# Kernel optimization log

Measured on AMD Instinct MI355X. Metric: run time of the kernel, lower is better.

## Reference

```python
import math
import jax, jax.numpy as jnp
import numpy as np

# ---- module hyperparameters (from init_kwargs) ----
MAX_DISP = 48
IMG_WIDTH = 1248
W = IMG_WIDTH // 4          # 312 rows of the OT problem (left pixels)
C_COLS = MAX_DISP + W       # 360 columns (shifted right pixels)
NUM_ITER = 10
TAU = 0.95
EPS = 1.0
KAPPA = (1.0 - TAU) / 2.0
XI = (1.0 - TAU) / (1.0 + TAU)
RHO = EPS * TAU / (1.0 - TAU)
BIG_COST = 10000.0

B, H = 2, 64


def setup_inputs() -> dict:
    key = jax.random.key(0)
    scores = jax.random.normal(key, (B, MAX_DISP, H, W), dtype=jnp.float32)
    return {"scores": scores}


def _masked(x):
    # torch.where(isfinite(x), x, 0)
    return jnp.where(jnp.isfinite(x), x, jnp.zeros_like(x))


def _lse_kernel(Cm, f, g, axis):
    # S = (C - f[...,None] - g[...,None,:]) / eps ; eps*logsumexp(-S, axis)
    S = (Cm - f[..., None] - g[..., None, :]) / EPS
    w_res = EPS * jax.nn.logsumexp(-S, axis=axis)
    w_sgn = f if axis == -1 else g
    return w_res - _masked(w_sgn)


def _sinkhorn_update(Cm, f, g, axis, log_marginal):
    app = _lse_kernel(Cm, f, g, axis)
    return EPS * log_marginal - _masked(app)


def _smin(h, log_marginal):
    return -RHO * jax.nn.logsumexp(-h / RHO + log_marginal, axis=-1)


def _unbalanced_ot(Cm):
    # Cm: (B,H,W,C_COLS) cost matrix
    log_a = jnp.full((W,), -math.log(W), dtype=Cm.dtype)
    log_b = jnp.full((C_COLS,), -math.log(C_COLS), dtype=Cm.dtype)

    f = -EPS * jax.nn.logsumexp(-Cm / EPS + log_b, axis=-1)          # (B,H,W)
    g = jnp.zeros(Cm.shape[:2] + (C_COLS,), dtype=Cm.dtype)          # (B,H,C)

    for _ in range(NUM_ITER):
        old_f = f
        new_g = TAU * _sinkhorn_update(Cm, old_f, g, axis=-2, log_marginal=log_b)
        new_g = new_g - KAPPA * _smin(old_f, log_a)[..., None]
        new_g = new_g + XI * _smin(new_g, log_b)[..., None]
        new_f = TAU * _sinkhorn_update(Cm, f, new_g, axis=-1, log_marginal=log_a)
        new_f = new_f - KAPPA * _smin(new_g, log_b)[..., None]
        new_f = new_f + XI * _smin(new_f, log_a)[..., None]
        f, g = new_f, new_g

    S = (Cm - f[..., None] - g[..., None, :]) / EPS
    return jnp.exp(-S)                                               # transport plan P


def _scatter_to_cost(scores):
    # (B,D,H,W) scores -> (B,H,W,C_COLS) cost, vectorized scatter over d
    Bn, D, Hn, Wn = scores.shape
    j = jnp.arange(Wn)
    d = jnp.arange(D)
    col = j[None, :] - d[:, None] + MAX_DISP                          # (D,W), all in-range, no collisions
    jj = jnp.broadcast_to(j[None, :], (D, Wn))
    cost = jnp.full((Bn, Hn, Wn, C_COLS), BIG_COST, dtype=scores.dtype)
    # scores (B,D,H,W) -> (B,H,D,W) to match fancy-index result shape
    cost = cost.at[:, :, jj, col].set(-jnp.transpose(scores, (0, 2, 1, 3)))
    return cost


def _plan_to_disparity(P, D):
    right = jnp.arange(C_COLS, dtype=P.dtype) - D
    left = jnp.arange(W, dtype=P.dtype)
    disp_map = left[:, None] - right[None, :]                         # (W,C)
    mass = jnp.clip(jnp.sum(P, axis=-1), 1e-8, None)                  # (B,H,W)
    disp = jnp.sum(P * disp_map, axis=-1) / mass                      # (B,H,W)
    return disp[:, None, :, :]                                        # (B,1,H,W)


def reference(scores):
    D = scores.shape[1]
    Cm = _scatter_to_cost(scores)
    P = _unbalanced_ot(Cm)
    return _plan_to_disparity(P, D)
```

## Files before the change

kernel.cpp:

```cpp
#include <hip/hip_runtime.h>
#include <math.h>


#define MAXD   48
#define WROWS  312
#define CCOLS  360
#define NITER  10
#define NT     768
#define KD     24
#define NPHASE (2 * NITER + 1)

__device__ __forceinline__ float pair_sum(float x) {
    int y = __builtin_amdgcn_update_dpp(0, __float_as_int(x), 0xB1, 0xf, 0xf, true);
    return x + __int_as_float(y);
}

template <int CTRL>
__device__ __forceinline__ float dpp_add(float x, float acc) {
    int y = __builtin_amdgcn_update_dpp(0, __float_as_int(x), CTRL, 0xf, 0xf, true);
    return acc + __int_as_float(y);
}

__device__ __forceinline__ float dpp_sum64(float x) {
    x = dpp_add<0x111>(x, x);
    x = dpp_add<0x112>(x, x);
    x = dpp_add<0x114>(x, x);
    x = dpp_add<0x118>(x, x);
    x = dpp_add<0x142>(x, x);
    x = dpp_add<0x143>(x, x);
    return x;
}

__global__ __launch_bounds__(NT)
void ot_disp_kernel(const float* __restrict__ scores, float* __restrict__ out) {
    const int bid  = blockIdx.x;
    const int tid  = threadIdx.x;
    const int half = tid >> 1;
    const int sub  = tid & 1;

    const float LOG_A2 = -8.285402f;
    const float LOG_B2 = -8.491853f;
    const float TAU    = 0.95f;
    const float KAPPA  = 0.025f;
    const float XI     = 0.025641026f;
    const float RHO    = 19.0f;
    const float INVRHO = 0.052631579f;

    __shared__ float s_Eb[MAXD + WROWS + MAXD];
    __shared__ float s_G[CCOLS];
    __shared__ float s_acc[NPHASE];
    float* const s_E = s_Eb + MAXD;

    const bool rowAct = (half < WROWS);
    const bool colAct = (half >= 1 && half < CCOLS);

    const int b = bid >> 6, h = bid & 63;
    const float* src = scores + ((size_t)b * MAXD * 64 + h) * WROWS;
    const size_t dstr = (size_t)64 * WROWS;

    if (tid < NPHASE) s_acc[tid] = 0.0f;
    if (tid < MAXD) { s_Eb[tid] = 0.0f; s_Eb[MAXD + WROWS + tid] = 0.0f; }

    const int d0 = sub * KD;
    const int jb = (colAct ? half : 0) - MAXD + d0;
    const int jr = rowAct ? half : 0;
    const int gb = jr + MAXD - d0;

    float wrow[KD];
    float wcol[KD];
    #pragma unroll
    for (int k = 0; k < KD; ++k) {
        wrow[k] = __expf(src[dstr * (d0 + k) + jr]);
        int j = jb + k;
        bool v = colAct && ((unsigned)j < (unsigned)WROWS);
        float sv = src[dstr * (d0 + k) + (v ? j : 0)];
        wcol[k] = v ? __expf(sv) : 0.0f;
    }
    __syncthreads();

    float sminF;
    {
        float e0=0,e1=0,e2=0,e3=0;
        #pragma unroll
        for (int k = 0; k < KD; k += 4) {
            e0 += wrow[k]; e1 += wrow[k+1]; e2 += wrow[k+2]; e3 += wrow[k+3];
        }
        float s = pair_sum((e0+e1)+(e2+e3));
        float f2 = -LOG_B2 - __builtin_amdgcn_logf(s);
        bool own = rowAct && (sub == 0);
        if (own) s_E[half] = __builtin_amdgcn_exp2f(f2);
        float xs = own ? __builtin_amdgcn_exp2f(-f2 * INVRHO + LOG_A2) : 0.0f;
        float t = dpp_sum64(xs);
        if ((tid & 63) == 63) atomicAdd(&s_acc[0], t);
        __syncthreads();
        sminF = -RHO * __builtin_amdgcn_logf(s_acc[0]);
    }

    float wv = 0.0f, gshift = 0.0f, fshift = 0.0f;
    for (int it = 0; it < NITER; ++it) {
        float e0=0,e1=0,e2=0,e3=0;
        #pragma unroll
        for (int k = 0; k < KD; k += 4) {
            e0 = fmaf(wcol[k],   s_E[jb+k],   e0);
            e1 = fmaf(wcol[k+1], s_E[jb+k+1], e1);
            e2 = fmaf(wcol[k+2], s_E[jb+k+2], e2);
            e3 = fmaf(wcol[k+3], s_E[jb+k+3], e3);
        }
        float cs = pair_sum((e0+e1)+(e2+e3));
        float Cg = TAU * (LOG_B2 - fshift) - KAPPA * sminF;
        float vc = Cg - TAU * __builtin_amdgcn_logf(cs);
        bool ownC = colAct && (sub == 0);
        if (ownC) s_G[half] = __builtin_amdgcn_exp2f(vc);
        float xs = ownC ? __builtin_amdgcn_exp2f(-vc * INVRHO + LOG_B2) : 0.0f;
        float tg = dpp_sum64(xs);
        if ((tid & 63) == 63) atomicAdd(&s_acc[1 + 2*it], tg);
        __syncthreads();
        float sg = -RHO * __builtin_amdgcn_logf(s_acc[1 + 2*it]);
        gshift = XI * sg;
        float sminG = (1.0f + XI) * sg;

        float f0=0,f1=0,f2=0,f3=0;
        #pragma unroll
        for (int k = 0; k < KD; k += 4) {
            f0 = fmaf(wrow[k],   s_G[gb-k],   f0);
            f1 = fmaf(wrow[k+1], s_G[gb-k-1], f1);
            f2 = fmaf(wrow[k+2], s_G[gb-k-2], f2);
            f3 = fmaf(wrow[k+3], s_G[gb-k-3], f3);
        }
        float rs = pair_sum((f0+f1)+(f2+f3));
        float Cf = TAU * (LOG_A2 - gshift) - KAPPA * sminG;
        wv = Cf - TAU * __builtin_amdgcn_logf(rs);
        bool ownR = rowAct && (sub == 0);
        if (ownR) s_E[half] = __builtin_amdgcn_exp2f(wv);
        float xf = ownR ? __builtin_amdgcn_exp2f(-wv * INVRHO + LOG_A2) : 0.0f;
        float tf = dpp_sum64(xf);
        if ((tid & 63) == 63) atomicAdd(&s_acc[2 + 2*it], tf);
        __syncthreads();
        float sf = -RHO * __builtin_amdgcn_logf(s_acc[2 + 2*it]);
        fshift = XI * sf;
        sminF = (1.0f + XI) * sf;
    }

    float num = 0.0f, den = 0.0f;
    if (rowAct) {
        float d0a=0,d1a=0,n0=0,n1=0;
        #pragma unroll
        for (int k = 0; k < KD; k += 2) {
            float p0 = wrow[k]   * s_G[gb-k];
            float p1 = wrow[k+1] * s_G[gb-k-1];
            d0a += p0; d1a += p1;
            n0 += (float)(d0 + k)     * p0;
            n1 += (float)(d0 + k + 1) * p1;
        }
        den = d0a + d1a; num = n0 + n1;
    }
    den = pair_sum(den);
    num = pair_sum(num);
    if (rowAct && sub == 0) {
        float E = __builtin_amdgcn_exp2f(wv + fshift + gshift);
        float mass = fmaxf(E * den, 1e-8f);
        out[(size_t)bid * WROWS + half] = (E * num) / mass;
    }
}

extern "C" void kernel_launch(void* const* d_in, const int* in_sizes, int n_in,
                              void* d_out, int out_size, void* d_ws, size_t ws_size,
                              hipStream_t stream) {
    const float* scores = (const float*)d_in[0];
    float* out = (float*)d_out;
    ot_disp_kernel<<<128, NT, 0, stream>>>(scores, out);
}
```

Measured before the change: 26.35 us.

## Defer scalar shift recurrences to end and use float2 double-buffered LDS loads

The per-iteration scalar shifts (smin terms, gshift/fshift) are factored out of the exponentiated potentials, so the inner loop only stores normalized exp values and accumulates the logsumexp sums. The scalar recurrence is replayed once after the loop from the stored accumulators. This shortens the serial dependency chain after each barrier. Shared arrays are duplicated into even/odd-offset float2 copies so each thread can issue aligned 64-bit LDS reads regardless of parity, and the final pass reuses cached G values in registers. In exchange it adds LDS writes and more register pressure.

```diff
diff --git a/kernel.cpp b/kernel.cpp
--- a/kernel.cpp
+++ b/kernel.cpp
@@ -8,19 +8,17 @@
 #define NITER  10
 #define NT     768
 #define KD     24
-#define NPHASE (2 * NITER + 1)
+#define NACC   (2 * NITER + 1)
 
 __device__ __forceinline__ float pair_sum(float x) {
     int y = __builtin_amdgcn_update_dpp(0, __float_as_int(x), 0xB1, 0xf, 0xf, true);
     return x + __int_as_float(y);
 }
-
 template <int CTRL>
 __device__ __forceinline__ float dpp_add(float x, float acc) {
     int y = __builtin_amdgcn_update_dpp(0, __float_as_int(x), CTRL, 0xf, 0xf, true);
     return acc + __int_as_float(y);
 }
-
 __device__ __forceinline__ float dpp_sum64(float x) {
     x = dpp_add<0x111>(x, x);
     x = dpp_add<0x112>(x, x);
@@ -38,126 +36,142 @@
     const int half = tid >> 1;
     const int sub  = tid & 1;
 
-    const float LOG_A2 = -8.285402f;
-    const float LOG_B2 = -8.491853f;
+    const float LOG_A2 = -8.2854022f;
+    const float LOG_B2 = -8.4918531f;
     const float TAU    = 0.95f;
     const float KAPPA  = 0.025f;
     const float XI     = 0.025641026f;
     const float RHO    = 19.0f;
     const float INVRHO = 0.052631579f;
+    const float TIR    = 0.05f;
 
-    __shared__ float s_Eb[MAXD + WROWS + MAXD];
-    __shared__ float s_G[CCOLS];
-    __shared__ float s_acc[NPHASE];
-    float* const s_E = s_Eb + MAXD;
+    __shared__ float2 sEA[204], sEB[205], sGA[180], sGB[181];
+    __shared__ float  s_acc[NACC];
+    float* const EAf = (float*)sEA;  float* const EBf = (float*)sEB;
+    float* const GAf = (float*)sGA;  float* const GBf = (float*)sGB;
+
+    if (tid < 205) {
+        sEB[tid] = make_float2(0.f, 0.f);
+        if (tid < 204) sEA[tid] = make_float2(0.f, 0.f);
+        if (tid < 181) sGB[tid] = make_float2(0.f, 0.f);
+        if (tid < 180) sGA[tid] = make_float2(0.f, 0.f);
+    }
+    if (tid < NACC) s_acc[tid] = 0.f;
 
     const bool rowAct = (half < WROWS);
     const bool colAct = (half >= 1 && half < CCOLS);
+    const int b = bid >> 6, h = bid & 63;
+    const float* src = scores + ((size_t)(b * MAXD) * 64 + h) * WROWS;
+    const size_t dstr = (size_t)64 * WROWS;
+    const int d0 = sub * KD;
+    const int jr = rowAct ? half : 0;
+    const int jc = colAct ? half : 0;
 
-    const int b = bid >> 6, h = bid & 63;
-    const float* src = scores + ((size_t)b * MAXD * 64 + h) * WROWS;
-    const size_t dstr = (size_t)64 * WROWS;
+    float wcol[KD];
+    float wrowR[KD];
+    #pragma unroll
+    for (int m = 0; m < KD; ++m) {
+        wrowR[m] = __expf(src[dstr * (size_t)(d0 + 23 - m) + jr]);
+        int j = jc - MAXD + d0 + m;
+        bool v = colAct && ((unsigned)j < (unsigned)WROWS);
+        float sv = src[dstr * (size_t)(d0 + m) + (v ? j : 0)];
+        wcol[m] = v ? __expf(sv) : 0.0f;
+    }
 
-    if (tid < NPHASE) s_acc[tid] = 0.0f;
-    if (tid < MAXD) { s_Eb[tid] = 0.0f; s_Eb[MAXD + WROWS + tid] = 0.0f; }
+    const int pe = jc + d0;
+    const float2* const ep = (pe & 1) ? (sEB + ((pe + 1) >> 1)) : (sEA + (pe >> 1));
+    const int qg = jr + 25 - d0;
+    const float2* const gp = (qg & 1) ? (sGB + ((qg + 1) >> 1)) : (sGA + (qg >> 1));
 
-    const int d0 = sub * KD;
-    const int jb = (colAct ? half : 0) - MAXD + d0;
-    const int jr = rowAct ? half : 0;
-    const int gb = jr + MAXD - d0;
-
-    float wrow[KD];
-    float wcol[KD];
-    #pragma unroll
-    for (int k = 0; k < KD; ++k) {
-        wrow[k] = __expf(src[dstr * (d0 + k) + jr]);
-        int j = jb + k;
-        bool v = colAct && ((unsigned)j < (unsigned)WROWS);
-        float sv = src[dstr * (d0 + k) + (v ? j : 0)];
-        wcol[k] = v ? __expf(sv) : 0.0f;
-    }
     __syncthreads();
 
-    float sminF;
     {
-        float e0=0,e1=0,e2=0,e3=0;
+        float a0=0,a1=0,a2=0,a3=0;
         #pragma unroll
-        for (int k = 0; k < KD; k += 4) {
-            e0 += wrow[k]; e1 += wrow[k+1]; e2 += wrow[k+2]; e3 += wrow[k+3];
+        for (int m = 0; m < KD; m += 4) {
+            a0 += wrowR[m];   a1 += wrowR[m+1];
+            a2 += wrowR[m+2]; a3 += wrowR[m+3];
         }
-        float s = pair_sum((e0+e1)+(e2+e3));
-        float f2 = -LOG_B2 - __builtin_amdgcn_logf(s);
+        float s  = pair_sum((a0 + a1) + (a2 + a3));
+        float ls = __builtin_amdgcn_logf(s);
+        float eh = __builtin_amdgcn_exp2f(-ls);
         bool own = rowAct && (sub == 0);
-        if (own) s_E[half] = __builtin_amdgcn_exp2f(f2);
-        float xs = own ? __builtin_amdgcn_exp2f(-f2 * INVRHO + LOG_A2) : 0.0f;
-        float t = dpp_sum64(xs);
+        if (own) { EAf[half + MAXD] = eh; EBf[half + MAXD + 1] = eh; }
+        float yv = __builtin_amdgcn_exp2f(fmaf(INVRHO, ls, LOG_A2));
+        float t  = dpp_sum64(own ? yv : 0.0f);
         if ((tid & 63) == 63) atomicAdd(&s_acc[0], t);
         __syncthreads();
-        sminF = -RHO * __builtin_amdgcn_logf(s_acc[0]);
     }
 
-    float wv = 0.0f, gshift = 0.0f, fshift = 0.0f;
+    float2 gv[12];
+    float ehat = 0.f, den = 0.f;
     for (int it = 0; it < NITER; ++it) {
-        float e0=0,e1=0,e2=0,e3=0;
+        float a0=0,a1=0,a2=0,a3=0;
         #pragma unroll
-        for (int k = 0; k < KD; k += 4) {
-            e0 = fmaf(wcol[k],   s_E[jb+k],   e0);
-            e1 = fmaf(wcol[k+1], s_E[jb+k+1], e1);
-            e2 = fmaf(wcol[k+2], s_E[jb+k+2], e2);
-            e3 = fmaf(wcol[k+3], s_E[jb+k+3], e3);
+        for (int u = 0; u < 12; u += 2) {
+            float2 v0 = ep[u], v1 = ep[u+1];
+            a0 = fmaf(wcol[2*u],   v0.x, a0);
+            a1 = fmaf(wcol[2*u+1], v0.y, a1);
+            a2 = fmaf(wcol[2*u+2], v1.x, a2);
+            a3 = fmaf(wcol[2*u+3], v1.y, a3);
         }
-        float cs = pair_sum((e0+e1)+(e2+e3));
-        float Cg = TAU * (LOG_B2 - fshift) - KAPPA * sminF;
-        float vc = Cg - TAU * __builtin_amdgcn_logf(cs);
+        float cs  = pair_sum((a0 + a1) + (a2 + a3));
+        float lcs = __builtin_amdgcn_logf(cs);
+        float gh  = __builtin_amdgcn_exp2f(-TAU * lcs);
         bool ownC = colAct && (sub == 0);
-        if (ownC) s_G[half] = __builtin_amdgcn_exp2f(vc);
-        float xs = ownC ? __builtin_amdgcn_exp2f(-vc * INVRHO + LOG_B2) : 0.0f;
-        float tg = dpp_sum64(xs);
+        if (ownC) { GAf[half] = gh; GBf[half + 1] = gh; }
+        float yv = __builtin_amdgcn_exp2f(fmaf(TIR, lcs, LOG_B2));
+        float tg = dpp_sum64(ownC ? yv : 0.0f);
         if ((tid & 63) == 63) atomicAdd(&s_acc[1 + 2*it], tg);
         __syncthreads();
-        float sg = -RHO * __builtin_amdgcn_logf(s_acc[1 + 2*it]);
-        gshift = XI * sg;
-        float sminG = (1.0f + XI) * sg;
 
-        float f0=0,f1=0,f2=0,f3=0;
+        float b0=0,b1=0,b2=0,b3=0;
         #pragma unroll
-        for (int k = 0; k < KD; k += 4) {
-            f0 = fmaf(wrow[k],   s_G[gb-k],   f0);
-            f1 = fmaf(wrow[k+1], s_G[gb-k-1], f1);
-            f2 = fmaf(wrow[k+2], s_G[gb-k-2], f2);
-            f3 = fmaf(wrow[k+3], s_G[gb-k-3], f3);
+        for (int u = 0; u < 12; u += 2) {
+            gv[u] = gp[u]; gv[u+1] = gp[u+1];
+            b0 = fmaf(wrowR[2*u],   gv[u].x,   b0);
+            b1 = fmaf(wrowR[2*u+1], gv[u].y,   b1);
+            b2 = fmaf(wrowR[2*u+2], gv[u+1].x, b2);
+            b3 = fmaf(wrowR[2*u+3], gv[u+1].y, b3);
         }
-        float rs = pair_sum((f0+f1)+(f2+f3));
-        float Cf = TAU * (LOG_A2 - gshift) - KAPPA * sminG;
-        wv = Cf - TAU * __builtin_amdgcn_logf(rs);
+        den = pair_sum((b0 + b1) + (b2 + b3));
+        float lrs = __builtin_amdgcn_logf(den);
+        ehat = __builtin_amdgcn_exp2f(-TAU * lrs);
         bool ownR = rowAct && (sub == 0);
-        if (ownR) s_E[half] = __builtin_amdgcn_exp2f(wv);
-        float xf = ownR ? __builtin_amdgcn_exp2f(-wv * INVRHO + LOG_A2) : 0.0f;
-        float tf = dpp_sum64(xf);
+        if (ownR) { EAf[half + MAXD] = ehat; EBf[half + MAXD + 1] = ehat; }
+        float yf = __builtin_amdgcn_exp2f(fmaf(TIR, lrs, LOG_A2));
+        float tf = dpp_sum64(ownR ? yf : 0.0f);
         if ((tid & 63) == 63) atomicAdd(&s_acc[2 + 2*it], tf);
         __syncthreads();
-        float sf = -RHO * __builtin_amdgcn_logf(s_acc[2 + 2*it]);
-        fshift = XI * sf;
+    }
+
+    float R[NACC];
+    #pragma unroll
+    for (int t = 0; t < NACC; ++t) R[t] = __builtin_amdgcn_logf(s_acc[t]);
+    float fsh   = -LOG_B2;
+    float sminF = fsh - RHO * R[0];
+    float gsh   = 0.f;
+    #pragma unroll
+    for (int it = 0; it < NITER; ++it) {
+        float Cg = TAU * (LOG_B2 - fsh) - KAPPA * sminF;
+        float sg = Cg - RHO * R[1 + 2*it];
+        gsh = Cg + XI * sg;
+        float sminG = (1.0f + XI) * sg;
+        float Cf = TAU * (LOG_A2 - gsh) - KAPPA * sminG;
+        float sf = Cf - RHO * R[2 + 2*it];
+        fsh   = Cf + XI * sf;
         sminF = (1.0f + XI) * sf;
     }
 
-    float num = 0.0f, den = 0.0f;
-    if (rowAct) {
-        float d0a=0,d1a=0,n0=0,n1=0;
-        #pragma unroll
-        for (int k = 0; k < KD; k += 2) {
-            float p0 = wrow[k]   * s_G[gb-k];
-            float p1 = wrow[k+1] * s_G[gb-k-1];
-            d0a += p0; d1a += p1;
-            n0 += (float)(d0 + k)     * p0;
-            n1 += (float)(d0 + k + 1) * p1;
-        }
-        den = d0a + d1a; num = n0 + n1;
+    float n0 = 0.f, n1 = 0.f;
+    #pragma unroll
+    for (int u = 0; u < 12; ++u) {
+        n0 = fmaf((float)(d0 + 23 - 2*u) * wrowR[2*u],   gv[u].x, n0);
+        n1 = fmaf((float)(d0 + 22 - 2*u) * wrowR[2*u+1], gv[u].y, n1);
     }
-    den = pair_sum(den);
-    num = pair_sum(num);
+    float num = pair_sum(n0 + n1);
     if (rowAct && sub == 0) {
-        float E = __builtin_amdgcn_exp2f(wv + fshift + gshift);
+        float E = __builtin_amdgcn_exp2f(fsh + gsh) * ehat;
         float mass = fmaxf(E * den, 1e-8f);
         out[(size_t)bid * WROWS + half] = (E * num) / mass;
     }
```

New measurement: 25.98 us. Within noise of the previous version (-1.4%).
